# Optimization experiments

Measured on AMD Instinct MI355X. Metric: run time of the kernel, lower is better.

Reference implementation:

```python
import jax, jax.numpy as jnp
import numpy as np

B, S, D, H = 2, 2048, 1024, 16
DH = D // H  # 64

def setup_inputs() -> dict:
    key = jax.random.key(0)
    ks = jax.random.split(key, 11)
    sc = 1.0 / np.sqrt(D)
    return {
        "query": jax.random.normal(ks[0], (B, S, D), jnp.float32),
        "key":   jax.random.normal(ks[1], (B, S, D), jnp.float32),
        "value": jax.random.normal(ks[2], (B, S, D), jnp.float32),
        "Wq": jax.random.normal(ks[3], (D, D), jnp.float32) * sc,
        "bq": jnp.zeros((D,), jnp.float32),
        "Wk": jax.random.normal(ks[4], (D, D), jnp.float32) * sc,
        "bk": jnp.zeros((D,), jnp.float32),
        "Wv": jax.random.normal(ks[5], (D, D), jnp.float32) * sc,
        "bv": jnp.zeros((D,), jnp.float32),
        "Wo": jax.random.normal(ks[6], (D, D), jnp.float32) * sc,
        "bo": jnp.zeros((D,), jnp.float32),
    }

def reference(query, key, value, Wq, bq, Wk, bk, Wv, bv, Wo, bo):
    # torch Linear: y = x @ W^T + b
    def split_heads(x):  # (B,S,D) -> (B,H,S,DH)
        return x.reshape(B, S, H, DH).transpose(0, 2, 1, 3)
    Q = split_heads(query @ Wq.T + bq)
    K = split_heads(key   @ Wk.T + bk)
    V = split_heads(value @ Wv.T + bv)
    scores = jnp.einsum('bhqd,bhkd->bhqk', Q, K) / jnp.sqrt(jnp.float32(DH))
    # Original applies torch.softmax(scores, dim=1) on a (B*H, Sq, Sk) tensor,
    # i.e. normalization over the QUERY axis -> axis=-2 here (faithful to source).
    attn = jax.nn.softmax(scores, axis=-2)
    # dropout omitted for deterministic reference (identity / eval mode)
    out = jnp.einsum('bhqk,bhkd->bhqd', attn, V)  # (B,H,S,DH)
    out = out.transpose(0, 2, 1, 3).reshape(B, S, D)
    return out @ Wo.T + bo
```

## Files before the change

### kernel.cpp

```cpp
#include <hip/hip_runtime.h>
#include <hip/hip_bf16.h>
#include <math.h>

#define BB 2
#define SS 2048
#define DD 1024
#define HH 16
#define DH 64

typedef __bf16 bf16;
typedef __bf16 bf16x8 __attribute__((ext_vector_type(8)));
typedef __bf16 bf16x4 __attribute__((ext_vector_type(4)));
typedef short short4v __attribute__((ext_vector_type(4)));
typedef float f32x4 __attribute__((ext_vector_type(4)));

static const size_t NTOK  = (size_t)BB * SS * DD;


__device__ __forceinline__ f32x4 mfma16(bf16x8 a, bf16x8 b, f32x4 c) {
    return __builtin_amdgcn_mfma_f32_16x16x32_bf16(a, b, c, 0, 0, 0);
}
__device__ __forceinline__ f32x4 mfma16k16(short4v a, short4v b, f32x4 c) {
    return __builtin_amdgcn_mfma_f32_16x16x16bf16_1k(a, b, c, 0, 0, 0);
}

__device__ __forceinline__ void gload_lds16(const void* g, void* l) {
    __builtin_amdgcn_global_load_lds(
        (const __attribute__((address_space(1))) void*)g,
        (__attribute__((address_space(3))) void*)l, 16, 0, 0);
}

__device__ __forceinline__ bf16x8 cvt8(float4 a, float4 b) {
    bf16x8 r;
    r[0] = (bf16)a.x; r[1] = (bf16)a.y; r[2] = (bf16)a.z; r[3] = (bf16)a.w;
    r[4] = (bf16)b.x; r[5] = (bf16)b.y; r[6] = (bf16)b.z; r[7] = (bf16)b.w;
    return r;
}

__global__ void signal_f(float* out, float v) {
    if (threadIdx.x == 0 && blockIdx.x == 0) out[0] = v;
}

#define LDP3 40

__global__ __launch_bounds__(256, 3) void qkv3(
    const float* __restrict__ Aq, const float* __restrict__ Ak,
    const float* __restrict__ Av,
    const float* __restrict__ Wq, const float* __restrict__ bq,
    const float* __restrict__ Wk, const float* __restrict__ bk,
    const float* __restrict__ Wv, const float* __restrict__ bv,
    bf16* __restrict__ Qs, bf16* __restrict__ Ks, bf16* __restrict__ Vt)
{
    const int K = DD, N = DD;
    __shared__ bf16 As[2][128][LDP3];
    __shared__ bf16 Bs[2][128][LDP3];

    int t = (int)threadIdx.x;
    int lane = t & 63, w = t >> 6;
    int wm = w >> 1, wn = w & 1;
    int c16 = lane & 15, quad = lane >> 4, ko = quad << 3;

    int x = blockIdx.x & 7;
    int j = blockIdx.x >> 3;
    int proj = j % 3;
    int jj = j / 3;
    int tm = x + ((jj >> 3) << 3);
    int tn = jj & 7;

    const float* A    = (proj == 0) ? Aq : (proj == 1) ? Ak : Av;
    const float* W    = (proj == 0) ? Wq : (proj == 1) ? Wk : Wv;
    const float* bias = (proj == 0) ? bq : (proj == 1) ? bk : bv;
    bf16*        C    = (proj == 0) ? Qs : (proj == 1) ? Ks : Vt;
    float osc = (proj == 0) ? 0.125f : 1.0f;

    int arow = t >> 1, acb = (t & 1) * 16;
    const float* abase = A + (size_t)(tm * 128 + arow) * K + acb;
    const float* wbase = W + (size_t)(tn * 128 + arow) * K + acb;

    f32x4 acc[4][4];
#pragma unroll
    for (int i = 0; i < 4; ++i)
#pragma unroll
        for (int q = 0; q < 4; ++q) acc[i][q] = (f32x4){0.f, 0.f, 0.f, 0.f};

    float4 av0, av1, av2, av3, wv0, wv1, wv2, wv3;
    av0 = *(const float4*)(abase);     av1 = *(const float4*)(abase + 4);
    av2 = *(const float4*)(abase + 8); av3 = *(const float4*)(abase + 12);
    wv0 = *(const float4*)(wbase);     wv1 = *(const float4*)(wbase + 4);
    wv2 = *(const float4*)(wbase + 8); wv3 = *(const float4*)(wbase + 12);
    *(bf16x8*)&As[0][arow][acb]     = cvt8(av0, av1);
    *(bf16x8*)&As[0][arow][acb + 8] = cvt8(av2, av3);
    *(bf16x8*)&Bs[0][arow][acb]     = cvt8(wv0, wv1);
    *(bf16x8*)&Bs[0][arow][acb + 8] = cvt8(wv2, wv3);
    __syncthreads();

    int bi = 0;
    for (int k0 = 0; k0 < K; k0 += 32) {
        int kn = k0 + 32;
        if (kn < K) {
            av0 = *(const float4*)(abase + kn);
            av1 = *(const float4*)(abase + kn + 4);
            av2 = *(const float4*)(abase + kn + 8);
            av3 = *(const float4*)(abase + kn + 12);
            wv0 = *(const float4*)(wbase + kn);
            wv1 = *(const float4*)(wbase + kn + 4);
            wv2 = *(const float4*)(wbase + kn + 8);
            wv3 = *(const float4*)(wbase + kn + 12);
        }
        bf16x8 af[4], bfr[4];
#pragma unroll
        for (int mt = 0; mt < 4; ++mt)
            af[mt] = *(const bf16x8*)&As[bi][wm * 64 + mt * 16 + c16][ko];
#pragma unroll
        for (int nt = 0; nt < 4; ++nt)
            bfr[nt] = *(const bf16x8*)&Bs[bi][wn * 64 + nt * 16 + c16][ko];
#pragma unroll
        for (int mt = 0; mt < 4; ++mt)
#pragma unroll
            for (int nt = 0; nt < 4; ++nt)
                acc[mt][nt] = mfma16(af[mt], bfr[nt], acc[mt][nt]);

        if (kn < K) {
            *(bf16x8*)&As[bi ^ 1][arow][acb]     = cvt8(av0, av1);
            *(bf16x8*)&As[bi ^ 1][arow][acb + 8] = cvt8(av2, av3);
            *(bf16x8*)&Bs[bi ^ 1][arow][acb]     = cvt8(wv0, wv1);
            *(bf16x8*)&Bs[bi ^ 1][arow][acb + 8] = cvt8(wv2, wv3);
        }
        __syncthreads();
        bi ^= 1;
    }

#pragma unroll
    for (int nt = 0; nt < 4; ++nt) {
        int col = tn * 128 + wn * 64 + nt * 16 + c16;
        float bv = bias[col];
#pragma unroll
        for (int mt = 0; mt < 4; ++mt) {
            int r0 = tm * 128 + wm * 64 + mt * 16 + quad * 4;
            if (proj == 2) {
                int b2 = r0 >> 11;
                int s  = r0 & (SS - 1);
                size_t base = ((size_t)b2 * N + col) * SS + s;
                bf16x4 pk;
#pragma unroll
                for (int r = 0; r < 4; ++r)
                    pk[r] = (bf16)(acc[mt][nt][r] + bv);
                *(bf16x4*)&C[base] = pk;
            } else {
#pragma unroll
                for (int r = 0; r < 4; ++r)
                    C[(size_t)(r0 + r) * N + col] =
                        (bf16)((acc[mt][nt][r] + bv) * osc);
            }
        }
    }
}

__global__ __launch_bounds__(256) void gemm3(
    const bf16* __restrict__ A, const float* __restrict__ W,
    const float* __restrict__ bias, float* __restrict__ C)
{
    const int K = DD, N = DD;
    __shared__ bf16 As[2][128][32];
    __shared__ bf16 Bs[2][128][32];

    int t = (int)threadIdx.x;
    int lane = t & 63, w = t >> 6;
    int wm = w >> 1, wn = w & 1;
    int c16 = lane & 15, quad = lane >> 4, ko = quad << 3;

    int x = blockIdx.x & 7, j = blockIdx.x >> 3;
    int tm = x + ((j >> 3) << 3);
    int tn = j & 7;

    int ar = w * 32 + (lane >> 2);
    int ac = (lane & 3) * 8;
    const bf16* agsrc = A + (size_t)(tm * 128 + ar) * K + ac;

    int wrow = t >> 1, wcb = (t & 1) * 16;
    const float* wsrc = W + (size_t)(tn * 128 + wrow) * K + wcb;

    f32x4 acc[4][4];
#pragma unroll
    for (int i = 0; i < 4; ++i)
#pragma unroll
        for (int jj = 0; jj < 4; ++jj) acc[i][jj] = (f32x4){0.f, 0.f, 0.f, 0.f};

    float4 wv0, wv1, wv2, wv3;
#pragma unroll
    for (int i = 0; i < 2; ++i)
        gload_lds16(agsrc + (size_t)(i * 16) * K, &As[0][w * 32 + i * 16][0]);
    wv0 = *(const float4*)(wsrc);
    wv1 = *(const float4*)(wsrc + 4);
    wv2 = *(const float4*)(wsrc + 8);
    wv3 = *(const float4*)(wsrc + 12);
    *(bf16x8*)&Bs[0][wrow][wcb]     = cvt8(wv0, wv1);
    *(bf16x8*)&Bs[0][wrow][wcb + 8] = cvt8(wv2, wv3);
    __syncthreads();

    int bi = 0;
    for (int k0 = 0; k0 < K; k0 += 32) {
        int kn = k0 + 32;
        if (kn < K) {
#pragma unroll
            for (int i = 0; i < 2; ++i)
                gload_lds16(agsrc + (size_t)(i * 16) * K + kn,
                            &As[bi ^ 1][w * 32 + i * 16][0]);
            wv0 = *(const float4*)(wsrc + kn);
            wv1 = *(const float4*)(wsrc + kn + 4);
            wv2 = *(const float4*)(wsrc + kn + 8);
            wv3 = *(const float4*)(wsrc + kn + 12);
        }
        bf16x8 af[4], bfr[4];
#pragma unroll
        for (int mt = 0; mt < 4; ++mt)
            af[mt] = *(const bf16x8*)&As[bi][wm * 64 + mt * 16 + c16][ko];
#pragma unroll
        for (int nt = 0; nt < 4; ++nt)
            bfr[nt] = *(const bf16x8*)&Bs[bi][wn * 64 + nt * 16 + c16][ko];
#pragma unroll
        for (int mt = 0; mt < 4; ++mt)
#pragma unroll
            for (int nt = 0; nt < 4; ++nt)
                acc[mt][nt] = mfma16(af[mt], bfr[nt], acc[mt][nt]);

        if (kn < K) {
            *(bf16x8*)&Bs[bi ^ 1][wrow][wcb]     = cvt8(wv0, wv1);
            *(bf16x8*)&Bs[bi ^ 1][wrow][wcb + 8] = cvt8(wv2, wv3);
        }
        __syncthreads();
        bi ^= 1;
    }

#pragma unroll
    for (int nt = 0; nt < 4; ++nt) {
        int col = tn * 128 + wn * 64 + nt * 16 + c16;
        float bv = bias[col];
#pragma unroll
        for (int mt = 0; mt < 4; ++mt) {
            int r0 = tm * 128 + wm * 64 + mt * 16 + quad * 4;
#pragma unroll
            for (int r = 0; r < 4; ++r)
                C[(size_t)(r0 + r) * N + col] = acc[mt][nt][r] + bv;
        }
    }
}

__global__ __launch_bounds__(512) void col_stats3(
    const bf16* __restrict__ Q, const bf16* __restrict__ Km,
    float* __restrict__ rzS)
{
    __shared__ __align__(16) bf16 Qlds[2][32][64];

    int t = (int)threadIdx.x;
    int w = t >> 6, lane = t & 63;
    int c16 = lane & 15, quad = lane >> 4, ko = quad << 3;

    int x = blockIdx.x & 7, j = blockIdx.x >> 3;
    int bh = ((j >> 3) << 3) + x;
    int kg = j & 7;
    int b = bh >> 4, h = bh & (HH - 1);
    int kbase = kg * 256 + w * 32;

    bf16x8 kf[2][2];
#pragma unroll
    for (int g = 0; g < 2; ++g) {
        const bf16* kp =
            Km + ((size_t)(b * SS + kbase + g * 16 + c16)) * DD + h * DH + ko;
        kf[g][0] = *(const bf16x8*)kp;
        kf[g][1] = *(const bf16x8*)(kp + 32);
    }

    int srow  = ((w & 3) << 3) + (lane >> 3);
    int schnk = (lane & 7) ^ (srow & 7);
    const bf16* gsrc = Q + ((size_t)(b * SS + srow)) * DD + h * DH + schnk * 8;
    int ldsOff = (w & 3) << 10;
    bool stager = (w < 4);

    float z[2][4] = {{0.f,0.f,0.f,0.f},{0.f,0.f,0.f,0.f}};

    int bi = 0;
    if (stager) gload_lds16(gsrc, (char*)&Qlds[0][0][0] + ldsOff);
    __syncthreads();

    for (int q0 = 0; q0 < SS; q0 += 32) {
        if (q0 + 32 < SS && stager)
            gload_lds16(gsrc + (size_t)(q0 + 32) * DD,
                        (char*)&Qlds[bi ^ 1][0][0] + ldsOff);
        const char* ql = (const char*)&Qlds[bi][0][0];
#pragma unroll
        for (int qs = 0; qs < 2; ++qs) {
            int row = qs * 16 + c16;
            int p0  = quad ^ (row & 7);
            bf16x8 qf0 = *(const bf16x8*)(ql + row * 128 + p0 * 16);
            bf16x8 qf1 = *(const bf16x8*)(ql + row * 128 + (p0 ^ 4) * 16);
#pragma unroll
            for (int g = 0; g < 2; ++g) {
                f32x4 a = {0.f, 0.f, 0.f, 0.f};
                a = mfma16(kf[g][0], qf0, a);
                a = mfma16(kf[g][1], qf1, a);
#pragma unroll
                for (int r = 0; r < 4; ++r)
                    z[g][r] += __expf(a[r]);
            }
        }
        __syncthreads();
        bi ^= 1;
    }

#pragma unroll
    for (int g = 0; g < 2; ++g)
#pragma unroll
        for (int r = 0; r < 4; ++r) {
#pragma unroll
            for (int off = 1; off < 16; off <<= 1)
                z[g][r] += __shfl_xor(z[g][r], off, 64);
        }
    if (c16 == 0) {
        size_t base = (size_t)bh * SS + kbase + quad * 4;
#pragma unroll
        for (int g = 0; g < 2; ++g)
#pragma unroll
            for (int r = 0; r < 4; ++r)
                rzS[base + g * 16 + r] = 1.0f / z[g][r];
    }
}

__global__ __launch_bounds__(512) void attn_ctx5(
    const bf16* __restrict__ Q, const bf16* __restrict__ Km,
    const bf16* __restrict__ Vt, const float* __restrict__ rzS,
    bf16* __restrict__ ctx)
{
    __shared__ __align__(16) char lds[2][8192];

    int t = (int)threadIdx.x;
    int w = t >> 6, lane = t & 63;
    int c16 = lane & 15, quad = lane >> 4, ko = quad << 3;

    int bid = blockIdx.x;
    int x = bid & 7, j = bid >> 3;
    int bh = ((j >> 3) << 3) + x;
    int qg = j & 7;
    int b = bh >> 4, h = bh & (HH - 1);
    int qt0 = qg * 16 + w * 2;

    const bf16* qp0 = Q + ((size_t)(b * SS + qt0 * 16 + c16)) * DD + h * DH + ko;
    bf16x8 qa0 = *(const bf16x8*)qp0;
    bf16x8 qa1 = *(const bf16x8*)(qp0 + 32);
    const bf16* qp1 = qp0 + (size_t)16 * DD;
    bf16x8 qb0 = *(const bf16x8*)qp1;
    bf16x8 qb1 = *(const bf16x8*)(qp1 + 32);

    const bf16* gsrc;
    int ldsOff;
    if (w < 4) {
        int row   = (w << 3) + (lane >> 3);
        int chunk = (lane & 7) ^ (row & 7);
        gsrc  = Km + ((size_t)(b * SS + row)) * DD + h * DH + chunk * 8;
        ldsOff = (w << 10);
    } else {
        int i = w - 4;
        int row   = (i << 4) + (lane >> 2);
        int chunk = (lane & 3) ^ (row & 3);
        gsrc  = Vt + ((size_t)(b * DD + h * DH + row)) * SS + chunk * 8;
        ldsOff = 4096 + (i << 10);
    }

    int kread  = c16 * 128 + ((quad ^ (c16 & 7)) << 4);
    int vread0 = c16 * 64 + (((quad >> 1) ^ (c16 & 3)) << 4) + ((quad & 1) << 3);

    const float* rzp = rzS + (size_t)bh * SS + quad * 4;

    f32x4 oa[4] = {{0,0,0,0},{0,0,0,0},{0,0,0,0},{0,0,0,0}};
    f32x4 ob[4] = {{0,0,0,0},{0,0,0,0},{0,0,0,0},{0,0,0,0}};

    int bi = 0;
    gload_lds16(gsrc, &lds[0][ldsOff]);
    __syncthreads();

    for (int kb = 0; kb < SS; kb += 32) {
        if (kb + 32 < SS) {
            const bf16* g = (w < 4) ? gsrc + (size_t)(kb + 32) * DD
                                    : gsrc + (kb + 32);
            gload_lds16(g, &lds[bi ^ 1][ldsOff]);
        }
        const char* kl = &lds[bi][0];
        const char* vl = &lds[bi][4096];
#pragma unroll
        for (int ks = 0; ks < 2; ++ks) {
            int kb0 = kread + ks * 2048;
            bf16x8 kf0 = *(const bf16x8*)(kl + kb0);
            bf16x8 kf1 = *(const bf16x8*)(kl + (kb0 ^ 64));
            f32x4 z4 = *(const f32x4*)(rzp + kb + ks * 16);
            f32x4 sa = {0,0,0,0}, sb = {0,0,0,0};
            sa = mfma16(kf0, qa0, sa);
            sa = mfma16(kf1, qa1, sa);
            sb = mfma16(kf0, qb0, sb);
            sb = mfma16(kf1, qb1, sb);

            union { bf16x4 b; short4v s; } pa, pb;
#pragma unroll
            for (int r = 0; r < 4; ++r) {
                pa.b[r] = (bf16)(__expf(sa[r]) * z4[r]);
                pb.b[r] = (bf16)(__expf(sb[r]) * z4[r]);
            }
            int vb0 = ks ? (vread0 ^ 32) : vread0;
#pragma unroll
            for (int dt = 0; dt < 4; ++dt) {
                short4v vf = *(const short4v*)(vl + vb0 + dt * 1024);
                oa[dt] = mfma16k16(pa.s, vf, oa[dt]);
                ob[dt] = mfma16k16(pb.s, vf, ob[dt]);
            }
        }
        __syncthreads();
        bi ^= 1;
    }

    size_t orow = ((size_t)(b * SS + qt0 * 16 + quad * 4)) * DD + h * DH + c16;
#pragma unroll
    for (int dt = 0; dt < 4; ++dt)
#pragma unroll
        for (int r = 0; r < 4; ++r) {
            ctx[orow + (size_t)r * DD + dt * 16] = (bf16)oa[dt][r];
            ctx[orow + (size_t)(16 + r) * DD + dt * 16] = (bf16)ob[dt][r];
        }
}

extern "C" void kernel_launch(void* const* d_in, const int* in_sizes, int n_in,
                              void* d_out, int out_size, void* d_ws, size_t ws_size,
                              hipStream_t stream) {
    const float* query = (const float*)d_in[0];
    const float* key   = (const float*)d_in[1];
    const float* value = (const float*)d_in[2];
    const float* Wq = (const float*)d_in[3];
    const float* bq = (const float*)d_in[4];
    const float* Wk = (const float*)d_in[5];
    const float* bk = (const float*)d_in[6];
    const float* Wv = (const float*)d_in[7];
    const float* bv = (const float*)d_in[8];
    const float* Wo = (const float*)d_in[9];
    const float* bo = (const float*)d_in[10];
    float* out = (float*)d_out;

    if (n_in != 11 || in_sizes[0] != (int)NTOK || in_sizes[3] != DD * DD ||
        in_sizes[4] != DD || out_size != (int)NTOK) {
        hipLaunchKernelGGL(signal_f, dim3(1), dim3(64), 0, stream, out, -64.0f);
        return;
    }

    bf16* Qs  = (bf16*)d_ws;
    bf16* Ks  = Qs + NTOK;
    bf16* Vt  = Ks + NTOK;
    bf16* Cs  = Vt + NTOK;
    float* rzS = (float*)(Cs + NTOK);

    hipLaunchKernelGGL(qkv3, dim3(768), dim3(256), 0, stream,
                       query, key, value, Wq, bq, Wk, bk, Wv, bv, Qs, Ks, Vt);

    hipLaunchKernelGGL(col_stats3, dim3(256), dim3(512), 0, stream, Qs, Ks, rzS);

    hipLaunchKernelGGL(attn_ctx5, dim3(256), dim3(512), 0, stream,
                       Qs, Ks, Vt, rzS, Cs);

    hipLaunchKernelGGL(gemm3, dim3(256), dim3(256), 0, stream, Cs, Wo, bo, out);
}
```

Before: 306.3 us.

## Pre-convert weights to bf16 and deepen async LDS pipelines with vmcnt waits

```diff
diff --git a/kernel.cpp b/kernel.cpp
--- a/kernel.cpp
+++ b/kernel.cpp
@@ -23,13 +23,11 @@
 __device__ __forceinline__ f32x4 mfma16k16(short4v a, short4v b, f32x4 c) {
     return __builtin_amdgcn_mfma_f32_16x16x16bf16_1k(a, b, c, 0, 0, 0);
 }
-
 __device__ __forceinline__ void gload_lds16(const void* g, void* l) {
     __builtin_amdgcn_global_load_lds(
         (const __attribute__((address_space(1))) void*)g,
         (__attribute__((address_space(3))) void*)l, 16, 0, 0);
 }
-
 __device__ __forceinline__ bf16x8 cvt8(float4 a, float4 b) {
     bf16x8 r;
     r[0] = (bf16)a.x; r[1] = (bf16)a.y; r[2] = (bf16)a.z; r[3] = (bf16)a.w;
@@ -37,18 +35,43 @@
     return r;
 }
 
+#define WAITV(N)  asm volatile("s_waitcnt vmcnt(" #N ")" ::: "memory")
+#define BAR()     __builtin_amdgcn_s_barrier()
+
 __global__ void signal_f(float* out, float v) {
     if (threadIdx.x == 0 && blockIdx.x == 0) out[0] = v;
 }
 
+__global__ __launch_bounds__(256) void cvt_bf16(
+    const float* __restrict__ s, bf16* __restrict__ d)
+{
+    size_t i = ((size_t)blockIdx.x * 256 + threadIdx.x) * 8;
+    float4 a = *(const float4*)(s + i);
+    float4 b = *(const float4*)(s + i + 4);
+    *(bf16x8*)(d + i) = cvt8(a, b);
+}
+__global__ __launch_bounds__(256) void cvt_w3(
+    const float* __restrict__ w0, const float* __restrict__ w1,
+    const float* __restrict__ w2, bf16* __restrict__ o0,
+    bf16* __restrict__ o1, bf16* __restrict__ o2)
+{
+    const float* s = (blockIdx.y == 0) ? w0 : (blockIdx.y == 1) ? w1 : w2;
+    bf16*        d = (blockIdx.y == 0) ? o0 : (blockIdx.y == 1) ? o1 : o2;
+    size_t i = ((size_t)blockIdx.x * 256 + threadIdx.x) * 8;
+    float4 a = *(const float4*)(s + i);
+    float4 b = *(const float4*)(s + i + 4);
+    *(bf16x8*)(d + i) = cvt8(a, b);
+}
+
 #define LDP3 40
 
-__global__ __launch_bounds__(256, 3) void qkv3(
+__global__ __launch_bounds__(256, 3) void qkv4(
     const float* __restrict__ Aq, const float* __restrict__ Ak,
     const float* __restrict__ Av,
-    const float* __restrict__ Wq, const float* __restrict__ bq,
-    const float* __restrict__ Wk, const float* __restrict__ bk,
-    const float* __restrict__ Wv, const float* __restrict__ bv,
+    const bf16* __restrict__ Wqb, const bf16* __restrict__ Wkb,
+    const bf16* __restrict__ Wvb,
+    const float* __restrict__ bq, const float* __restrict__ bk,
+    const float* __restrict__ bv,
     bf16* __restrict__ Qs, bf16* __restrict__ Ks, bf16* __restrict__ Vt)
 {
     const int K = DD, N = DD;
@@ -62,20 +85,20 @@
 
     int x = blockIdx.x & 7;
     int j = blockIdx.x >> 3;
-    int proj = j % 3;
-    int jj = j / 3;
-    int tm = x + ((jj >> 3) << 3);
-    int tn = jj & 7;
+    int proj = j >> 5;
+    int rem  = j & 31;
+    int tm = x + ((rem >> 3) << 3);
+    int tn = rem & 7;
 
     const float* A    = (proj == 0) ? Aq : (proj == 1) ? Ak : Av;
-    const float* W    = (proj == 0) ? Wq : (proj == 1) ? Wk : Wv;
+    const bf16*  W    = (proj == 0) ? Wqb : (proj == 1) ? Wkb : Wvb;
     const float* bias = (proj == 0) ? bq : (proj == 1) ? bk : bv;
     bf16*        C    = (proj == 0) ? Qs : (proj == 1) ? Ks : Vt;
     float osc = (proj == 0) ? 0.125f : 1.0f;
 
     int arow = t >> 1, acb = (t & 1) * 16;
     const float* abase = A + (size_t)(tm * 128 + arow) * K + acb;
-    const float* wbase = W + (size_t)(tn * 128 + arow) * K + acb;
+    const bf16*  wbase = W + (size_t)(tn * 128 + arow) * K + acb;
 
     f32x4 acc[4][4];
 #pragma unroll
@@ -83,15 +106,16 @@
 #pragma unroll
         for (int q = 0; q < 4; ++q) acc[i][q] = (f32x4){0.f, 0.f, 0.f, 0.f};
 
-    float4 av0, av1, av2, av3, wv0, wv1, wv2, wv3;
+    float4 av0, av1, av2, av3;
+    bf16x8 wv0, wv1;
     av0 = *(const float4*)(abase);     av1 = *(const float4*)(abase + 4);
     av2 = *(const float4*)(abase + 8); av3 = *(const float4*)(abase + 12);
-    wv0 = *(const float4*)(wbase);     wv1 = *(const float4*)(wbase + 4);
-    wv2 = *(const float4*)(wbase + 8); wv3 = *(const float4*)(wbase + 12);
+    wv0 = *(const bf16x8*)(wbase);
+    wv1 = *(const bf16x8*)(wbase + 8);
     *(bf16x8*)&As[0][arow][acb]     = cvt8(av0, av1);
     *(bf16x8*)&As[0][arow][acb + 8] = cvt8(av2, av3);
-    *(bf16x8*)&Bs[0][arow][acb]     = cvt8(wv0, wv1);
-    *(bf16x8*)&Bs[0][arow][acb + 8] = cvt8(wv2, wv3);
+    *(bf16x8*)&Bs[0][arow][acb]     = wv0;
+    *(bf16x8*)&Bs[0][arow][acb + 8] = wv1;
     __syncthreads();
 
     int bi = 0;
@@ -102,10 +126,8 @@
             av1 = *(const float4*)(abase + kn + 4);
             av2 = *(const float4*)(abase + kn + 8);
             av3 = *(const float4*)(abase + kn + 12);
-            wv0 = *(const float4*)(wbase + kn);
-            wv1 = *(const float4*)(wbase + kn + 4);
-            wv2 = *(const float4*)(wbase + kn + 8);
-            wv3 = *(const float4*)(wbase + kn + 12);
+            wv0 = *(const bf16x8*)(wbase + kn);
+            wv1 = *(const bf16x8*)(wbase + kn + 8);
         }
         bf16x8 af[4], bfr[4];
 #pragma unroll
@@ -123,8 +145,8 @@
         if (kn < K) {
             *(bf16x8*)&As[bi ^ 1][arow][acb]     = cvt8(av0, av1);
             *(bf16x8*)&As[bi ^ 1][arow][acb + 8] = cvt8(av2, av3);
-            *(bf16x8*)&Bs[bi ^ 1][arow][acb]     = cvt8(wv0, wv1);
-            *(bf16x8*)&Bs[bi ^ 1][arow][acb + 8] = cvt8(wv2, wv3);
+            *(bf16x8*)&Bs[bi ^ 1][arow][acb]     = wv0;
+            *(bf16x8*)&Bs[bi ^ 1][arow][acb + 8] = wv1;
         }
         __syncthreads();
         bi ^= 1;
@@ -133,7 +155,7 @@
 #pragma unroll
     for (int nt = 0; nt < 4; ++nt) {
         int col = tn * 128 + wn * 64 + nt * 16 + c16;
-        float bv = bias[col];
+        float bv2 = bias[col];
 #pragma unroll
         for (int mt = 0; mt < 4; ++mt) {
             int r0 = tm * 128 + wm * 64 + mt * 16 + quad * 4;
@@ -144,25 +166,24 @@
                 bf16x4 pk;
 #pragma unroll
                 for (int r = 0; r < 4; ++r)
-                    pk[r] = (bf16)(acc[mt][nt][r] + bv);
+                    pk[r] = (bf16)(acc[mt][nt][r] + bv2);
                 *(bf16x4*)&C[base] = pk;
             } else {
 #pragma unroll
                 for (int r = 0; r < 4; ++r)
                     C[(size_t)(r0 + r) * N + col] =
-                        (bf16)((acc[mt][nt][r] + bv) * osc);
+                        (bf16)((acc[mt][nt][r] + bv2) * osc);
             }
         }
     }
 }
 
-__global__ __launch_bounds__(256) void gemm3(
-    const bf16* __restrict__ A, const float* __restrict__ W,
+__global__ __launch_bounds__(256) void gemm5(
+    const bf16* __restrict__ A, const bf16* __restrict__ W,
     const float* __restrict__ bias, float* __restrict__ C)
 {
-    const int K = DD, N = DD;
-    __shared__ bf16 As[2][128][32];
-    __shared__ bf16 Bs[2][128][32];
+    __shared__ __align__(16) bf16 As[4][128][32];
+    __shared__ __align__(16) bf16 Bs[4][128][32];
 
     int t = (int)threadIdx.x;
     int lane = t & 63, w = t >> 6;
@@ -173,63 +194,57 @@
     int tm = x + ((j >> 3) << 3);
     int tn = j & 7;
 
-    int ar = w * 32 + (lane >> 2);
-    int ac = (lane & 3) * 8;
-    const bf16* agsrc = A + (size_t)(tm * 128 + ar) * K + ac;
-
-    int wrow = t >> 1, wcb = (t & 1) * 16;
-    const float* wsrc = W + (size_t)(tn * 128 + wrow) * K + wcb;
+    int wr0 = lane >> 2;
+    int wsw = (lane & 3) ^ (wr0 & 3);
+    const bf16* asrc = A + (size_t)(tm * 128 + w * 32 + wr0) * DD + wsw * 8;
+    const bf16* wsrc = W + (size_t)(tn * 128 + w * 32 + wr0) * DD + wsw * 8;
+    char* adst = (char*)&As[0][0][0] + w * 2048;
+    char* wdst = (char*)&Bs[0][0][0] + w * 2048;
 
     f32x4 acc[4][4];
 #pragma unroll
     for (int i = 0; i < 4; ++i)
 #pragma unroll
-        for (int jj = 0; jj < 4; ++jj) acc[i][jj] = (f32x4){0.f, 0.f, 0.f, 0.f};
-
-    float4 wv0, wv1, wv2, wv3;
-#pragma unroll
-    for (int i = 0; i < 2; ++i)
-        gload_lds16(agsrc + (size_t)(i * 16) * K, &As[0][w * 32 + i * 16][0]);
-    wv0 = *(const float4*)(wsrc);
-    wv1 = *(const float4*)(wsrc + 4);
-    wv2 = *(const float4*)(wsrc + 8);
-    wv3 = *(const float4*)(wsrc + 12);
-    *(bf16x8*)&Bs[0][wrow][wcb]     = cvt8(wv0, wv1);
-    *(bf16x8*)&Bs[0][wrow][wcb + 8] = cvt8(wv2, wv3);
-    __syncthreads();
-
-    int bi = 0;
-    for (int k0 = 0; k0 < K; k0 += 32) {
-        int kn = k0 + 32;
-        if (kn < K) {
-#pragma unroll
-            for (int i = 0; i < 2; ++i)
-                gload_lds16(agsrc + (size_t)(i * 16) * K + kn,
-                            &As[bi ^ 1][w * 32 + i * 16][0]);
-            wv0 = *(const float4*)(wsrc + kn);
-            wv1 = *(const float4*)(wsrc + kn + 4);
-            wv2 = *(const float4*)(wsrc + kn + 8);
-            wv3 = *(const float4*)(wsrc + kn + 12);
-        }
+        for (int q = 0; q < 4; ++q) acc[i][q] = (f32x4){0.f, 0.f, 0.f, 0.f};
+
+#pragma unroll
+    for (int s = 0; s < 2; ++s) {
+        gload_lds16(asrc + s * 32, adst + s * 8192);
+        gload_lds16(asrc + (size_t)16 * DD + s * 32, adst + s * 8192 + 1024);
+        gload_lds16(wsrc + s * 32, wdst + s * 8192);
+        gload_lds16(wsrc + (size_t)16 * DD + s * 32, wdst + s * 8192 + 1024);
+    }
+
+    for (int t0 = 0; t0 < 32; ++t0) {
+        if (t0 + 2 < 32) {
+            int s = t0 + 2, sb = (s & 3) * 8192;
+            gload_lds16(asrc + s * 32, adst + sb);
+            gload_lds16(asrc + (size_t)16 * DD + s * 32, adst + sb + 1024);
+            gload_lds16(wsrc + s * 32, wdst + sb);
+            gload_lds16(wsrc + (size_t)16 * DD + s * 32, wdst + sb + 1024);
+        }
+        if (t0 < 30)      { WAITV(8); }
+        else if (t0 == 30){ WAITV(4); }
+        else              { WAITV(0); }
+        BAR();
+        const char* al = (const char*)&As[0][0][0] + (t0 & 3) * 8192;
+        const char* wl = (const char*)&Bs[0][0][0] + (t0 & 3) * 8192;
         bf16x8 af[4], bfr[4];
 #pragma unroll
-        for (int mt = 0; mt < 4; ++mt)
-            af[mt] = *(const bf16x8*)&As[bi][wm * 64 + mt * 16 + c16][ko];
-#pragma unroll
-        for (int nt = 0; nt < 4; ++nt)
-            bfr[nt] = *(const bf16x8*)&Bs[bi][wn * 64 + nt * 16 + c16][ko];
+        for (int mt = 0; mt < 4; ++mt) {
+            int row = wm * 64 + mt * 16 + c16;
+            af[mt] = *(const bf16x8*)(al + row * 64 + ((quad ^ (row & 3)) << 4));
+        }
+#pragma unroll
+        for (int nt = 0; nt < 4; ++nt) {
+            int row = wn * 64 + nt * 16 + c16;
+            bfr[nt] = *(const bf16x8*)(wl + row * 64 + ((quad ^ (row & 3)) << 4));
+        }
 #pragma unroll
         for (int mt = 0; mt < 4; ++mt)
 #pragma unroll
             for (int nt = 0; nt < 4; ++nt)
                 acc[mt][nt] = mfma16(af[mt], bfr[nt], acc[mt][nt]);
-
-        if (kn < K) {
-            *(bf16x8*)&Bs[bi ^ 1][wrow][wcb]     = cvt8(wv0, wv1);
-            *(bf16x8*)&Bs[bi ^ 1][wrow][wcb + 8] = cvt8(wv2, wv3);
-        }
-        __syncthreads();
-        bi ^= 1;
     }
 
 #pragma unroll
@@ -241,16 +256,16 @@
             int r0 = tm * 128 + wm * 64 + mt * 16 + quad * 4;
 #pragma unroll
             for (int r = 0; r < 4; ++r)
-                C[(size_t)(r0 + r) * N + col] = acc[mt][nt][r] + bv;
-        }
-    }
-}
-
-__global__ __launch_bounds__(512) void col_stats3(
+                C[(size_t)(r0 + r) * DD + col] = acc[mt][nt][r] + bv;
+        }
+    }
+}
+
+__global__ __launch_bounds__(512) void col_stats4(
     const bf16* __restrict__ Q, const bf16* __restrict__ Km,
     float* __restrict__ rzS)
 {
-    __shared__ __align__(16) bf16 Qlds[2][32][64];
+    __shared__ __align__(16) bf16 Qlds[4][32][64];
 
     int t = (int)threadIdx.x;
     int w = t >> 6, lane = t & 63;
@@ -279,15 +294,20 @@
 
     float z[2][4] = {{0.f,0.f,0.f,0.f},{0.f,0.f,0.f,0.f}};
 
-    int bi = 0;
-    if (stager) gload_lds16(gsrc, (char*)&Qlds[0][0][0] + ldsOff);
-    __syncthreads();
-
-    for (int q0 = 0; q0 < SS; q0 += 32) {
-        if (q0 + 32 < SS && stager)
-            gload_lds16(gsrc + (size_t)(q0 + 32) * DD,
-                        (char*)&Qlds[bi ^ 1][0][0] + ldsOff);
-        const char* ql = (const char*)&Qlds[bi][0][0];
+    if (stager) {
+        gload_lds16(gsrc, (char*)&Qlds[0][0][0] + ldsOff);
+        gload_lds16(gsrc + (size_t)32 * DD, (char*)&Qlds[1][0][0] + ldsOff);
+    }
+
+    for (int t0 = 0; t0 < 64; ++t0) {
+        if (t0 + 2 < 64 && stager)
+            gload_lds16(gsrc + (size_t)(t0 + 2) * 32 * DD,
+                        (char*)&Qlds[(t0 + 2) & 3][0][0] + ldsOff);
+        if (t0 < 62)      { WAITV(2); }
+        else if (t0 == 62){ WAITV(1); }
+        else              { WAITV(0); }
+        BAR();
+        const char* ql = (const char*)&Qlds[t0 & 3][0][0];
 #pragma unroll
         for (int qs = 0; qs < 2; ++qs) {
             int row = qs * 16 + c16;
@@ -304,8 +324,6 @@
                     z[g][r] += __expf(a[r]);
             }
         }
-        __syncthreads();
-        bi ^= 1;
     }
 
 #pragma unroll
@@ -326,12 +344,12 @@
     }
 }
 
-__global__ __launch_bounds__(512) void attn_ctx5(
+__global__ __launch_bounds__(512) void attn_ctx6(
     const bf16* __restrict__ Q, const bf16* __restrict__ Km,
     const bf16* __restrict__ Vt, const float* __restrict__ rzS,
     bf16* __restrict__ ctx)
 {
-    __shared__ __align__(16) char lds[2][8192];
+    __shared__ __align__(16) char lds[4][8192];
 
     int t = (int)threadIdx.x;
     int w = t >> 6, lane = t & 63;
@@ -353,7 +371,8 @@
 
     const bf16* gsrc;
     int ldsOff;
-    if (w < 4) {
+    bool isK = (w < 4);
+    if (isK) {
         int row   = (w << 3) + (lane >> 3);
         int chunk = (lane & 7) ^ (row & 7);
         gsrc  = Km + ((size_t)(b * SS + row)) * DD + h * DH + chunk * 8;
@@ -374,18 +393,22 @@
     f32x4 oa[4] = {{0,0,0,0},{0,0,0,0},{0,0,0,0},{0,0,0,0}};
     f32x4 ob[4] = {{0,0,0,0},{0,0,0,0},{0,0,0,0},{0,0,0,0}};
 
-    int bi = 0;
     gload_lds16(gsrc, &lds[0][ldsOff]);
-    __syncthreads();
-
-    for (int kb = 0; kb < SS; kb += 32) {
-        if (kb + 32 < SS) {
-            const bf16* g = (w < 4) ? gsrc + (size_t)(kb + 32) * DD
-                                    : gsrc + (kb + 32);
-            gload_lds16(g, &lds[bi ^ 1][ldsOff]);
-        }
-        const char* kl = &lds[bi][0];
-        const char* vl = &lds[bi][4096];
+    gload_lds16(isK ? gsrc + (size_t)32 * DD : gsrc + 32, &lds[1][ldsOff]);
+
+    for (int t0 = 0; t0 < 64; ++t0) {
+        if (t0 + 2 < 64) {
+            int s = t0 + 2;
+            const bf16* g = isK ? gsrc + (size_t)(s * 32) * DD : gsrc + s * 32;
+            gload_lds16(g, &lds[s & 3][ldsOff]);
+        }
+        if (t0 < 62)      { WAITV(2); }
+        else if (t0 == 62){ WAITV(1); }
+        else              { WAITV(0); }
+        BAR();
+        const char* kl = &lds[t0 & 3][0];
+        const char* vl = &lds[t0 & 3][4096];
+        int kb = t0 * 32;
 #pragma unroll
         for (int ks = 0; ks < 2; ++ks) {
             int kb0 = kread + ks * 2048;
@@ -412,8 +435,6 @@
                 ob[dt] = mfma16k16(pb.s, vf, ob[dt]);
             }
         }
-        __syncthreads();
-        bi ^= 1;
     }
 
     size_t orow = ((size_t)(b * SS + qt0 * 16 + quad * 4)) * DD + h * DH + c16;
@@ -454,13 +475,24 @@
     bf16* Cs  = Vt + NTOK;
     float* rzS = (float*)(Cs + NTOK);
 
-    hipLaunchKernelGGL(qkv3, dim3(768), dim3(256), 0, stream,
-                       query, key, value, Wq, bq, Wk, bk, Wv, bv, Qs, Ks, Vt);
-
-    hipLaunchKernelGGL(col_stats3, dim3(256), dim3(512), 0, stream, Qs, Ks, rzS);
-
-    hipLaunchKernelGGL(attn_ctx5, dim3(256), dim3(512), 0, stream,
+    bf16* Wqb = Cs;
+    bf16* Wkb = Cs + (size_t)DD * DD;
+    bf16* Wvb = Cs + (size_t)2 * DD * DD;
+    bf16* WoB = Qs;
+
+    hipLaunchKernelGGL(cvt_w3, dim3(512, 3), dim3(256), 0, stream,
+                       Wq, Wk, Wv, Wqb, Wkb, Wvb);
+
+    hipLaunchKernelGGL(qkv4, dim3(768), dim3(256), 0, stream,
+                       query, key, value, Wqb, Wkb, Wvb, bq, bk, bv,
+                       Qs, Ks, Vt);
+
+    hipLaunchKernelGGL(col_stats4, dim3(256), dim3(512), 0, stream, Qs, Ks, rzS);
+
+    hipLaunchKernelGGL(attn_ctx6, dim3(256), dim3(512), 0, stream,
                        Qs, Ks, Vt, rzS, Cs);
 
-    hipLaunchKernelGGL(gemm3, dim3(256), dim3(256), 0, stream, Cs, Wo, bo, out);
-}
+    hipLaunchKernelGGL(cvt_bf16, dim3(512), dim3(256), 0, stream, Wo, WoB);
+
+    hipLaunchKernelGGL(gemm5, dim3(256), dim3(256), 0, stream, Cs, WoB, bo, out);
+}
```

Result: faster. 288.8 us (-5.7%).
